# Optimization experiments

Measured on AMD Instinct MI355X. Metric: run time of the kernel, lower is better.

The kernel has to match this reference:

```python
import jax, jax.numpy as jnp
import numpy as np

D_MODEL = 1024
NUM_HEADS = 16
DEPTH = D_MODEL // NUM_HEADS
B, S = 2, 2048


def setup_inputs() -> dict:
    key = jax.random.key(0)
    ks = jax.random.split(key, 8)
    scale = 1.0 / np.sqrt(D_MODEL)
    return {
        "v": jax.random.normal(ks[0], (B, S, D_MODEL), jnp.float32),
        "k": jax.random.normal(ks[1], (B, S, D_MODEL), jnp.float32),
        "q": jax.random.normal(ks[2], (B, S, D_MODEL), jnp.float32),
        "mask": jnp.zeros((B, 1, 1, S), jnp.float32),
        "wq": jax.random.normal(ks[3], (D_MODEL, D_MODEL), jnp.float32) * scale,
        "wk": jax.random.normal(ks[4], (D_MODEL, D_MODEL), jnp.float32) * scale,
        "wv": jax.random.normal(ks[5], (D_MODEL, D_MODEL), jnp.float32) * scale,
        "wo": jax.random.normal(ks[6], (D_MODEL, D_MODEL), jnp.float32) * scale,
        "bq": jnp.zeros((D_MODEL,), jnp.float32),
        "bk": jnp.zeros((D_MODEL,), jnp.float32),
        "bv": jnp.zeros((D_MODEL,), jnp.float32),
        "bo": jnp.zeros((D_MODEL,), jnp.float32),
    }


def _split_heads(x):
    # [B, S, d_model] -> [B, H, S, depth]
    b, s, _ = x.shape
    return x.reshape(b, s, NUM_HEADS, DEPTH).transpose(0, 2, 1, 3)


def reference(v, k, q, mask, wq, wk, wv, wo, bq, bk, bv, bo):
    qh = _split_heads(q @ wq + bq)
    kh = _split_heads(k @ wk + bk)
    vh = _split_heads(v @ wv + bv)
    # scores: [B, H, Sq, Sk]
    scores = jnp.einsum("bhqd,bhkd->bhqk", qh, kh) / jnp.sqrt(
        jnp.asarray(DEPTH, jnp.float32))
    scores = scores + mask * -1e9
    attn = jax.nn.softmax(scores, axis=-1)
    out = jnp.einsum("bhqk,bhkd->bhqd", attn, vh)  # [B, H, Sq, depth]
    out = out.transpose(0, 2, 1, 3).reshape(q.shape[0], -1, D_MODEL)
    out = out @ wo + bo
    return out, attn
```

## Files before the change

kernel.cpp:

```cpp
#include <hip/hip_runtime.h>

#define S_LEN 2048
#define DM 1024
#define NH 16
#define DH 64

typedef __attribute__((ext_vector_type(8))) short short8;
typedef __attribute__((ext_vector_type(4))) float f32x4;
typedef __attribute__((ext_vector_type(16))) float f32x16;
typedef unsigned short u16;
typedef unsigned int u32;

__device__ __forceinline__ u16 f2b(float f){
  union { float f; u32 u; } v; v.f = f;
  return (u16)((v.u + 0x7fffu + ((v.u >> 16) & 1u)) >> 16);
}
__device__ __forceinline__ float b2f(u16 h){
  union { u32 u; float f; } v; v.u = ((u32)h) << 16; return v.f;
}

__device__ __forceinline__ f32x4 mfma16(short8 a, short8 b, f32x4 c){
  return __builtin_amdgcn_mfma_f32_16x16x32_bf16(a, b, c, 0, 0, 0);
}
__device__ __forceinline__ f32x16 mfma32(short8 a, short8 b, f32x16 c){
  return __builtin_amdgcn_mfma_f32_32x32x16_bf16(a, b, c, 0, 0, 0);
}

template<int R>
__device__ __forceinline__ void stage_tile(const u16* src, int ld, u16* lds){
  const int t = threadIdx.x;
  #pragma unroll
  for (int it = 0; it < R/32; ++it){
    int idx = it*256 + t;
    int row = idx >> 3;
    int ch  = (idx & 7) ^ (row & 7);
    const u16* g = src + row*ld + ch*8;
    u16* l = lds + (it*256 + (t & ~63))*8;
    __builtin_amdgcn_global_load_lds((const __attribute__((address_space(1))) void*)g,
                                     (__attribute__((address_space(3))) void*)l, 16, 0, 0);
  }
}

__device__ __forceinline__ short8 frag_ld(const u16* tile, int row, int ch){
  int off = (row*128 + ch*16) ^ ((row & 7) << 4);
  return *(const short8*)((const char*)tile + off);
}

__global__ __launch_bounds__(256) void k_cast(
    const float* __restrict__ q, const float* __restrict__ k, const float* __restrict__ v,
    u16* __restrict__ qb, u16* __restrict__ kb, u16* __restrict__ vb)
{
  int z = blockIdx.z;
  const float* src = (z==0)?q:(z==1)?k:v;
  u16* dst = (z==0)?qb:(z==1)?kb:vb;
  long i = ((long)blockIdx.x*256 + threadIdx.x)*8;
  f32x4 a = *(const f32x4*)(src + i);
  f32x4 b = *(const f32x4*)(src + i + 4);
  short8 o;
  #pragma unroll
  for (int j = 0; j < 4; ++j){ o[j] = (short)f2b(a[j]); o[4+j] = (short)f2b(b[j]); }
  *(short8*)(dst + i) = o;
}

__global__ __launch_bounds__(256) void k_transpose(
    const float* __restrict__ wq, const float* __restrict__ wk,
    const float* __restrict__ wv, const float* __restrict__ wo,
    u16* __restrict__ oq, u16* __restrict__ ok, u16* __restrict__ ov, u16* __restrict__ oo)
{
  int z = blockIdx.z;
  const float* W = (z==0)?wq:(z==1)?wk:(z==2)?wv:wo;
  u16* O = (z==0)?oq:(z==1)?ok:(z==2)?ov:oo;
  int k0 = blockIdx.x*64, n0 = blockIdx.y*64;
  __shared__ float tl[64][65];
  int t = threadIdx.x;
  #pragma unroll
  for (int i = 0; i < 16; ++i){
    int idx = i*256 + t;
    int row = idx >> 6, col = idx & 63;
    tl[row][col] = W[(long)(k0+row)*DM + n0 + col];
  }
  __syncthreads();
  #pragma unroll
  for (int i = 0; i < 16; ++i){
    int idx = i*256 + t;
    int n = idx >> 6, kk = idx & 63;
    O[(long)(n0+n)*DM + k0 + kk] = f2b(tl[kk][n]);
  }
}

__device__ __forceinline__ void gemm_body(const u16* __restrict__ X, const u16* __restrict__ WT,
    const float* __restrict__ bias, u16* __restrict__ dst16, float* __restrict__ dst32,
    int layout, int m0, int n0, u16* At, u16* Bt)
{
  const int t = threadIdx.x, lane = t & 63, w = t >> 6;
  const int wr = (w >> 1) * 64, wc = (w & 1) * 64;
  const int li = lane & 15, lg = lane >> 4;
  const f32x4 zero = {0.f, 0.f, 0.f, 0.f};
  f32x4 acc[4][4];
  #pragma unroll
  for (int m = 0; m < 4; ++m)
    #pragma unroll
    for (int n = 0; n < 4; ++n) acc[m][n] = zero;

  for (int kt = 0; kt < DM/64; ++kt){
    stage_tile<128>(X  + (long)m0*DM + kt*64, DM, At);
    stage_tile<128>(WT + (long)n0*DM + kt*64, DM, Bt);
    __syncthreads();
    #pragma unroll
    for (int ks = 0; ks < 2; ++ks){
      int ch = ks*4 + lg;
      short8 a[4], b[4];
      #pragma unroll
      for (int m = 0; m < 4; ++m) a[m] = frag_ld(At, wr + m*16 + li, ch);
      #pragma unroll
      for (int n = 0; n < 4; ++n) b[n] = frag_ld(Bt, wc + n*16 + li, ch);
      #pragma unroll
      for (int m = 0; m < 4; ++m)
        #pragma unroll
        for (int n = 0; n < 4; ++n) acc[m][n] = mfma16(a[m], b[n], acc[m][n]);
    }
    __syncthreads();
  }

  if (layout == 1){
    f32x4 bm[4];
    #pragma unroll
    for (int m = 0; m < 4; ++m) bm[m] = *(const f32x4*)(bias + m0 + wr + m*16 + lg*4);
    #pragma unroll
    for (int m = 0; m < 4; ++m)
      #pragma unroll
      for (int n = 0; n < 4; ++n)
        #pragma unroll
        for (int r = 0; r < 4; ++r){
          int gm = m0 + wr + m*16 + lg*4 + r;
          int gc = n0 + wc + n*16 + li;
          int hh = gm >> 6, dd = gm & 63, bb = gc >> 11, ss = gc & (S_LEN-1);
          dst16[(((long)(bb*NH + hh))*DH + dd)*S_LEN + ss] = f2b(acc[m][n][r] + bm[m][r]);
        }
  } else {
    float bv4[4];
    #pragma unroll
    for (int n = 0; n < 4; ++n) bv4[n] = bias[n0 + wc + n*16 + li];
    #pragma unroll
    for (int m = 0; m < 4; ++m)
      #pragma unroll
      for (int n = 0; n < 4; ++n)
        #pragma unroll
        for (int r = 0; r < 4; ++r){
          int gm = m0 + wr + m*16 + lg*4 + r;
          int gc = n0 + wc + n*16 + li;
          float val = acc[m][n][r] + bv4[n];
          if (layout == 0){
            int bb = gm >> 11, ss = gm & (S_LEN-1), hh = gc >> 6, dd = gc & 63;
            dst16[(((long)(bb*NH + hh))*S_LEN + ss)*DH + dd] = f2b(val);
          } else {
            dst32[(long)gm*DM + gc] = val;
          }
        }
  }
}

__global__ __launch_bounds__(256) void k_gemm_qkv(
    const u16* __restrict__ qb, const u16* __restrict__ kb, const u16* __restrict__ vb,
    const u16* __restrict__ wtq, const u16* __restrict__ wtk, const u16* __restrict__ wtv,
    const float* __restrict__ bq, const float* __restrict__ bk, const float* __restrict__ bv,
    u16* __restrict__ Qw, u16* __restrict__ Kw, u16* __restrict__ VTw)
{
  __shared__ u16 At[128*64], Bt[128*64];
  int bid = blockIdx.x;
  int xcd = bid & 7, j = bid >> 3;
  int z = j >> 5, tt = j & 31;
  int mi = xcd*4 + (tt >> 3), n = tt & 7;
  if (z == 2){
    gemm_body(wtv, vb, bv, VTw, nullptr, 1, n*128, mi*128, At, Bt);
  } else {
    const u16* X  = (z==0)?qb:kb;
    const u16* WT = (z==0)?wtq:wtk;
    const float* B = (z==0)?bq:bk;
    u16* dst = (z==0)?Qw:Kw;
    gemm_body(X, WT, B, dst, nullptr, 0, mi*128, n*128, At, Bt);
  }
}

__global__ __launch_bounds__(256) void k_gemm_out(
    const u16* __restrict__ ctx, const u16* __restrict__ wto,
    const float* __restrict__ bo, float* __restrict__ out)
{
  __shared__ u16 At[128*64], Bt[128*64];
  int bid = blockIdx.x;
  int xcd = bid & 7, tt = bid >> 3;
  int mi = xcd*4 + (tt >> 3), n = tt & 7;
  gemm_body(ctx, wto, bo, nullptr, out, 2, mi*128, n*128, At, Bt);
}

__global__ __launch_bounds__(256) void k_attn(const u16* __restrict__ Q, const u16* __restrict__ K,
    const u16* __restrict__ VT, const float* __restrict__ mask,
    float* __restrict__ attn, u16* __restrict__ ctx)
{
  __shared__ u16 Kt[2][64*64], Vt[2][64*64], Pt[128*64];
  const int t = threadIdx.x, lane = t & 63, w = t >> 6;
  const int lq = lane & 31, hi = lane >> 5;
  const int bid = blockIdx.x;
  const int bh = bid >> 4;
  const int q0 = (bid & 15) * 128;
  const int b = bh >> 4;
  const u16* Qb = Q + ((long)bh*S_LEN + q0 + w*32 + lq)*DH;
  short8 qa[4];
  #pragma unroll
  for (int ds = 0; ds < 4; ++ds) qa[ds] = *(const short8*)(Qb + ds*16 + hi*8);
  const float* mrow_g = mask + b*S_LEN;

  float lsum = 0.f;
  stage_tile<64>(K + (long)bh*S_LEN*DH, DH, Kt[0]);
  __syncthreads();
  for (int tt = 0; tt < S_LEN/64; ++tt){
    const u16* cur = Kt[tt & 1];
    if (tt + 1 < S_LEN/64)
      stage_tile<64>(K + ((long)bh*S_LEN + (tt+1)*64)*DH, DH, Kt[(tt+1) & 1]);
    #pragma unroll
    for (int kt = 0; kt < 2; ++kt){
      f32x16 acc = {};
      __builtin_amdgcn_s_setprio(1);
      #pragma unroll
      for (int ds = 0; ds < 4; ++ds)
        acc = mfma32(frag_ld(cur, kt*32 + lq, ds*2 + hi), qa[ds], acc);
      __builtin_amdgcn_s_setprio(0);
      #pragma unroll
      for (int rg = 0; rg < 4; ++rg){
        f32x4 mk = *(const f32x4*)(mrow_g + tt*64 + kt*32 + rg*8 + hi*4);
        #pragma unroll
        for (int j = 0; j < 4; ++j)
          lsum += __expf(acc[rg*4+j]*0.125f - 1e9f*mk[j]);
      }
    }
    __syncthreads();
  }
  lsum += __shfl_xor(lsum, 32);

  float rlw[8];
  #pragma unroll
  for (int i = 0; i < 8; ++i)
    rlw[i] = 1.f / __shfl(lsum, i*4 + (lane >> 4));

  f32x16 cacc[2] = {};
  const int prow = w*32 + lq;
  const int pswz = (prow & 7) << 4;

  stage_tile<64>(K  + (long)bh*S_LEN*DH, DH, Kt[0]);
  stage_tile<64>(VT + (long)bh*DH*S_LEN, S_LEN, Vt[0]);
  __syncthreads();
  for (int tt = 0; tt < S_LEN/64; ++tt){
    const int cur = tt & 1;
    if (tt + 1 < S_LEN/64){
      stage_tile<64>(K  + ((long)bh*S_LEN + (tt+1)*64)*DH, DH, Kt[cur^1]);
      stage_tile<64>(VT + (long)bh*DH*S_LEN + (tt+1)*64, S_LEN, Vt[cur^1]);
    }
    #pragma unroll
    for (int kt = 0; kt < 2; ++kt){
      f32x16 acc = {};
      __builtin_amdgcn_s_setprio(1);
      #pragma unroll
      for (int ds = 0; ds < 4; ++ds)
        acc = mfma32(frag_ld(Kt[cur], kt*32 + lq, ds*2 + hi), qa[ds], acc);
      __builtin_amdgcn_s_setprio(0);
      #pragma unroll
      for (int rg = 0; rg < 4; ++rg){
        f32x4 mk = *(const f32x4*)(mrow_g + tt*64 + kt*32 + rg*8 + hi*4);
        float p0 = __expf(acc[rg*4+0]*0.125f - 1e9f*mk[0]);
        float p1 = __expf(acc[rg*4+1]*0.125f - 1e9f*mk[1]);
        float p2 = __expf(acc[rg*4+2]*0.125f - 1e9f*mk[2]);
        float p3 = __expf(acc[rg*4+3]*0.125f - 1e9f*mk[3]);
        uint2 pu;
        pu.x = (u32)f2b(p0) | ((u32)f2b(p1) << 16);
        pu.y = (u32)f2b(p2) | ((u32)f2b(p3) << 16);
        int off = (prow*128 + (kt*32 + rg*8 + hi*4)*2) ^ pswz;
        *(uint2*)((char*)Pt + off) = pu;
      }
    }
    #pragma unroll
    for (int i = 0; i < 8; ++i){
      int rr = i*4 + (lane >> 4);
      int ch8 = lane & 15;
      int roff = ((w*32 + rr)*128 + ch8*8) ^ ((rr & 7) << 4);
      uint2 pr = *(const uint2*)((const char*)Pt + roff);
      f32x4 av;
      av[0] = b2f((u16)(pr.x & 0xffffu)) * rlw[i];
      av[1] = b2f((u16)(pr.x >> 16))     * rlw[i];
      av[2] = b2f((u16)(pr.y & 0xffffu)) * rlw[i];
      av[3] = b2f((u16)(pr.y >> 16))     * rlw[i];
      *(f32x4*)(attn + ((long)bh*S_LEN + q0 + w*32 + rr)*S_LEN + tt*64 + ch8*4) = av;
    }
    short8 pa[4];
    #pragma unroll
    for (int ks = 0; ks < 4; ++ks) pa[ks] = frag_ld(Pt, prow, ks*2 + hi);
    __builtin_amdgcn_s_setprio(1);
    #pragma unroll
    for (int dh = 0; dh < 2; ++dh)
      #pragma unroll
      for (int ks = 0; ks < 4; ++ks)
        cacc[dh] = mfma32(pa[ks], frag_ld(Vt[cur], dh*32 + lq, ks*2 + hi), cacc[dh]);
    __builtin_amdgcn_s_setprio(0);
    asm volatile("s_waitcnt vmcnt(8)" ::: "memory");
    __builtin_amdgcn_sched_barrier(0);
    __builtin_amdgcn_s_barrier();
  }

  int bb = bh >> 4, hh = bh & 15;
  #pragma unroll
  for (int r = 0; r < 16; ++r){
    int qrow = (r & 3) + 8*(r >> 2) + 4*hi;
    float rle = 1.f / __shfl(lsum, qrow);
    #pragma unroll
    for (int dh = 0; dh < 2; ++dh){
      float val = cacc[dh][r] * rle;
      ctx[((long)bb*S_LEN + q0 + w*32 + qrow)*DM + hh*DH + dh*32 + lq] = f2b(val);
    }
  }
}

extern "C" void kernel_launch(void* const* d_in, const int* in_sizes, int n_in,
                              void* d_out, int out_size, void* d_ws, size_t ws_size,
                              hipStream_t stream)
{
  const float* v_in = (const float*)d_in[0];
  const float* k_in = (const float*)d_in[1];
  const float* q_in = (const float*)d_in[2];
  const float* mask = (const float*)d_in[3];
  const float* wq = (const float*)d_in[4];
  const float* wk = (const float*)d_in[5];
  const float* wv = (const float*)d_in[6];
  const float* wo = (const float*)d_in[7];
  const float* bq = (const float*)d_in[8];
  const float* bk = (const float*)d_in[9];
  const float* bv = (const float*)d_in[10];
  const float* bo = (const float*)d_in[11];

  float* out  = (float*)d_out;
  float* attn = out + (long)2*S_LEN*DM;

  char* ws = (char*)d_ws;
  const long MW = 1024*1024;
  u16*  wtq = (u16*)(ws);
  u16*  wtk = (u16*)(ws + 2*MW);
  u16*  wtv = (u16*)(ws + 4*MW);
  u16*  wto = (u16*)(ws + 6*MW);
  u16*  qb  = (u16*)(ws + 8*MW);
  u16*  kb  = (u16*)(ws + 17*MW);
  u16*  vb  = (u16*)(ws + 26*MW);
  u16*  Qw  = (u16*)(ws + 35*MW);
  u16*  Kw  = (u16*)(ws + 44*MW);
  u16*  VTw = (u16*)(ws + 53*MW);
  u16*  ctx = (u16*)(ws + 8*MW);

  k_cast<<<dim3(2048,1,3), 256, 0, stream>>>(q_in, k_in, v_in, qb, kb, vb);
  k_transpose<<<dim3(16,16,4), 256, 0, stream>>>(wq,wk,wv,wo, wtq,wtk,wtv,wto);
  k_gemm_qkv<<<768, 256, 0, stream>>>(qb,kb,vb, wtq,wtk,wtv, bq,bk,bv, Qw,Kw,VTw);
  k_attn<<<512, 256, 0, stream>>>(Qw, Kw, VTw, mask, attn, ctx);
  k_gemm_out<<<256, 256, 0, stream>>>(ctx, wto, bo, out);
}
```

Measured before the change: 296.0 us.

## Load K/V fragments directly from global in attention, shrink blocks to two waves

The attention kernel no longer stages K and V tiles through shared memory with double buffering and barriers. Each wave now loads its MFMA fragments straight from global memory, relying on L2 for reuse. Blocks shrink to 128 threads covering 64 query rows, the grid doubles to 1024, and block ids are remapped so heads are grouped by XCD for L2 locality. This removes LDS traffic and block-wide syncs and raises occupancy, but each wave re-reads K/V from cache with less coalesced access and no explicit prefetch.

```diff
diff --git a/kernel.cpp b/kernel.cpp
--- a/kernel.cpp
+++ b/kernel.cpp
@@ -193,17 +193,20 @@
   gemm_body(ctx, wto, bo, nullptr, out, 2, mi*128, n*128, At, Bt);
 }
 
-__global__ __launch_bounds__(256) void k_attn(const u16* __restrict__ Q, const u16* __restrict__ K,
+__global__ __launch_bounds__(128) void k_attn(const u16* __restrict__ Q, const u16* __restrict__ K,
     const u16* __restrict__ VT, const float* __restrict__ mask,
     float* __restrict__ attn, u16* __restrict__ ctx)
 {
-  __shared__ u16 Kt[2][64*64], Vt[2][64*64], Pt[128*64];
+  __shared__ u16 Pt[64*64];
   const int t = threadIdx.x, lane = t & 63, w = t >> 6;
   const int lq = lane & 31, hi = lane >> 5;
   const int bid = blockIdx.x;
-  const int bh = bid >> 4;
-  const int q0 = (bid & 15) * 128;
+  const int xcd = bid & 7, j = bid >> 3;
+  const int bh = xcd + 8*(j & 3);
+  const int q0 = (j >> 2) * 64;
   const int b = bh >> 4;
+  const u16* Kb = K  + (long)bh*S_LEN*DH;
+  const u16* Vb = VT + (long)bh*DH*S_LEN;
   const u16* Qb = Q + ((long)bh*S_LEN + q0 + w*32 + lq)*DH;
   short8 qa[4];
   #pragma unroll
@@ -211,29 +214,26 @@
   const float* mrow_g = mask + b*S_LEN;
 
   float lsum = 0.f;
-  stage_tile<64>(K + (long)bh*S_LEN*DH, DH, Kt[0]);
-  __syncthreads();
   for (int tt = 0; tt < S_LEN/64; ++tt){
-    const u16* cur = Kt[tt & 1];
-    if (tt + 1 < S_LEN/64)
-      stage_tile<64>(K + ((long)bh*S_LEN + (tt+1)*64)*DH, DH, Kt[(tt+1) & 1]);
     #pragma unroll
     for (int kt = 0; kt < 2; ++kt){
+      short8 kf[4];
+      #pragma unroll
+      for (int ds = 0; ds < 4; ++ds)
+        kf[ds] = *(const short8*)(Kb + (long)(tt*64 + kt*32 + lq)*DH + ds*16 + hi*8);
       f32x16 acc = {};
       __builtin_amdgcn_s_setprio(1);
       #pragma unroll
-      for (int ds = 0; ds < 4; ++ds)
-        acc = mfma32(frag_ld(cur, kt*32 + lq, ds*2 + hi), qa[ds], acc);
+      for (int ds = 0; ds < 4; ++ds) acc = mfma32(kf[ds], qa[ds], acc);
       __builtin_amdgcn_s_setprio(0);
       #pragma unroll
       for (int rg = 0; rg < 4; ++rg){
         f32x4 mk = *(const f32x4*)(mrow_g + tt*64 + kt*32 + rg*8 + hi*4);
         #pragma unroll
-        for (int j = 0; j < 4; ++j)
-          lsum += __expf(acc[rg*4+j]*0.125f - 1e9f*mk[j]);
+        for (int jj = 0; jj < 4; ++jj)
+          lsum += __expf(acc[rg*4+jj]*0.125f - 1e9f*mk[jj]);
       }
     }
-    __syncthreads();
   }
   lsum += __shfl_xor(lsum, 32);
 
@@ -246,22 +246,17 @@
   const int prow = w*32 + lq;
   const int pswz = (prow & 7) << 4;
 
-  stage_tile<64>(K  + (long)bh*S_LEN*DH, DH, Kt[0]);
-  stage_tile<64>(VT + (long)bh*DH*S_LEN, S_LEN, Vt[0]);
-  __syncthreads();
   for (int tt = 0; tt < S_LEN/64; ++tt){
-    const int cur = tt & 1;
-    if (tt + 1 < S_LEN/64){
-      stage_tile<64>(K  + ((long)bh*S_LEN + (tt+1)*64)*DH, DH, Kt[cur^1]);
-      stage_tile<64>(VT + (long)bh*DH*S_LEN + (tt+1)*64, S_LEN, Vt[cur^1]);
-    }
     #pragma unroll
     for (int kt = 0; kt < 2; ++kt){
+      short8 kf[4];
+      #pragma unroll
+      for (int ds = 0; ds < 4; ++ds)
+        kf[ds] = *(const short8*)(Kb + (long)(tt*64 + kt*32 + lq)*DH + ds*16 + hi*8);
       f32x16 acc = {};
       __builtin_amdgcn_s_setprio(1);
       #pragma unroll
-      for (int ds = 0; ds < 4; ++ds)
-        acc = mfma32(frag_ld(Kt[cur], kt*32 + lq, ds*2 + hi), qa[ds], acc);
+      for (int ds = 0; ds < 4; ++ds) acc = mfma32(kf[ds], qa[ds], acc);
       __builtin_amdgcn_s_setprio(0);
       #pragma unroll
       for (int rg = 0; rg < 4; ++rg){
@@ -293,16 +288,19 @@
     short8 pa[4];
     #pragma unroll
     for (int ks = 0; ks < 4; ++ks) pa[ks] = frag_ld(Pt, prow, ks*2 + hi);
+    short8 vf[2][4];
+    #pragma unroll
+    for (int dh = 0; dh < 2; ++dh)
+      #pragma unroll
+      for (int ks = 0; ks < 4; ++ks)
+        vf[dh][ks] = *(const short8*)(Vb + (long)(dh*32 + lq)*S_LEN + tt*64 + ks*16 + hi*8);
     __builtin_amdgcn_s_setprio(1);
     #pragma unroll
     for (int dh = 0; dh < 2; ++dh)
       #pragma unroll
       for (int ks = 0; ks < 4; ++ks)
-        cacc[dh] = mfma32(pa[ks], frag_ld(Vt[cur], dh*32 + lq, ks*2 + hi), cacc[dh]);
+        cacc[dh] = mfma32(pa[ks], vf[dh][ks], cacc[dh]);
     __builtin_amdgcn_s_setprio(0);
-    asm volatile("s_waitcnt vmcnt(8)" ::: "memory");
-    __builtin_amdgcn_sched_barrier(0);
-    __builtin_amdgcn_s_barrier();
   }
 
   int bb = bh >> 4, hh = bh & 15;
@@ -355,6 +353,6 @@
   k_cast<<<dim3(2048,1,3), 256, 0, stream>>>(q_in, k_in, v_in, qb, kb, vb);
   k_transpose<<<dim3(16,16,4), 256, 0, stream>>>(wq,wk,wv,wo, wtq,wtk,wtv,wto);
   k_gemm_qkv<<<768, 256, 0, stream>>>(qb,kb,vb, wtq,wtk,wtv, bq,bk,bv, Qw,Kw,VTw);
-  k_attn<<<512, 256, 0, stream>>>(Qw, Kw, VTw, mask, attn, ctx);
+  k_attn<<<1024, 128, 0, stream>>>(Qw, Kw, VTw, mask, attn, ctx);
   k_gemm_out<<<256, 256, 0, stream>>>(ctx, wto, bo, out);
 }
```

Result: slower. 377.1 us (+27.4%).

## Process two 32-row query groups per wave to reuse K/V fragments in attention

Applied to the files above, without the earlier changes.

Each wave now computes 64 query rows as two 32-row groups, loading each K and V fragment from LDS once and feeding it into two MFMA chains. Block size in queries doubles, so the grid halves to 256 blocks, and blocks are remapped so each XCD serves a fixed set of heads for L2 locality. This cuts LDS fragment loads and K/V tile restaging per query, at the cost of more registers, a larger P buffer in LDS, and fewer resident blocks to hide memory latency.

```diff
diff --git a/kernel.cpp b/kernel.cpp
--- a/kernel.cpp
+++ b/kernel.cpp
@@ -197,20 +197,24 @@
     const u16* __restrict__ VT, const float* __restrict__ mask,
     float* __restrict__ attn, u16* __restrict__ ctx)
 {
-  __shared__ u16 Kt[2][64*64], Vt[2][64*64], Pt[128*64];
+  __shared__ u16 Kt[2][64*64], Vt[2][64*64], Pt[256*64];
   const int t = threadIdx.x, lane = t & 63, w = t >> 6;
   const int lq = lane & 31, hi = lane >> 5;
   const int bid = blockIdx.x;
-  const int bh = bid >> 4;
-  const int q0 = (bid & 15) * 128;
+  const int xcd = bid & 7, j = bid >> 3;
+  const int bh = xcd + 8*(j & 3);
+  const int q0 = (j >> 2) * 256;
   const int b = bh >> 4;
-  const u16* Qb = Q + ((long)bh*S_LEN + q0 + w*32 + lq)*DH;
-  short8 qa[4];
-  #pragma unroll
-  for (int ds = 0; ds < 4; ++ds) qa[ds] = *(const short8*)(Qb + ds*16 + hi*8);
+  short8 qa[2][4];
+  #pragma unroll
+  for (int g = 0; g < 2; ++g){
+    const u16* Qb = Q + ((long)bh*S_LEN + q0 + w*64 + g*32 + lq)*DH;
+    #pragma unroll
+    for (int ds = 0; ds < 4; ++ds) qa[g][ds] = *(const short8*)(Qb + ds*16 + hi*8);
+  }
   const float* mrow_g = mask + b*S_LEN;
 
-  float lsum = 0.f;
+  float lsum0 = 0.f, lsum1 = 0.f;
   stage_tile<64>(K + (long)bh*S_LEN*DH, DH, Kt[0]);
   __syncthreads();
   for (int tt = 0; tt < S_LEN/64; ++tt){
@@ -219,32 +223,42 @@
       stage_tile<64>(K + ((long)bh*S_LEN + (tt+1)*64)*DH, DH, Kt[(tt+1) & 1]);
     #pragma unroll
     for (int kt = 0; kt < 2; ++kt){
-      f32x16 acc = {};
+      short8 kf[4];
+      #pragma unroll
+      for (int ds = 0; ds < 4; ++ds) kf[ds] = frag_ld(cur, kt*32 + lq, ds*2 + hi);
+      f32x16 a0 = {}, a1 = {};
       __builtin_amdgcn_s_setprio(1);
       #pragma unroll
-      for (int ds = 0; ds < 4; ++ds)
-        acc = mfma32(frag_ld(cur, kt*32 + lq, ds*2 + hi), qa[ds], acc);
+      for (int ds = 0; ds < 4; ++ds) a0 = mfma32(kf[ds], qa[0][ds], a0);
+      #pragma unroll
+      for (int ds = 0; ds < 4; ++ds) a1 = mfma32(kf[ds], qa[1][ds], a1);
       __builtin_amdgcn_s_setprio(0);
       #pragma unroll
       for (int rg = 0; rg < 4; ++rg){
         f32x4 mk = *(const f32x4*)(mrow_g + tt*64 + kt*32 + rg*8 + hi*4);
         #pragma unroll
-        for (int j = 0; j < 4; ++j)
-          lsum += __expf(acc[rg*4+j]*0.125f - 1e9f*mk[j]);
+        for (int jj = 0; jj < 4; ++jj){
+          lsum0 += __expf(a0[rg*4+jj]*0.125f - 1e9f*mk[jj]);
+          lsum1 += __expf(a1[rg*4+jj]*0.125f - 1e9f*mk[jj]);
+        }
       }
     }
     __syncthreads();
   }
-  lsum += __shfl_xor(lsum, 32);
-
-  float rlw[8];
-  #pragma unroll
-  for (int i = 0; i < 8; ++i)
-    rlw[i] = 1.f / __shfl(lsum, i*4 + (lane >> 4));
-
-  f32x16 cacc[2] = {};
-  const int prow = w*32 + lq;
-  const int pswz = (prow & 7) << 4;
+  lsum0 += __shfl_xor(lsum0, 32);
+  lsum1 += __shfl_xor(lsum1, 32);
+
+  float rlw[16];
+  #pragma unroll
+  for (int i = 0; i < 16; ++i){
+    float ls = (i < 8) ? lsum0 : lsum1;
+    rlw[i] = 1.f / __shfl(ls, (i*4 + (lane >> 4)) & 31);
+  }
+
+  f32x16 cacc[2][2] = {};
+  const int prow0 = w*64 + lq;
+  const int prow1 = w*64 + 32 + lq;
+  const int pswz = (lq & 7) << 4;
 
   stage_tile<64>(K  + (long)bh*S_LEN*DH, DH, Kt[0]);
   stage_tile<64>(VT + (long)bh*DH*S_LEN, S_LEN, Vt[0]);
@@ -257,65 +271,94 @@
     }
     #pragma unroll
     for (int kt = 0; kt < 2; ++kt){
-      f32x16 acc = {};
+      short8 kf[4];
+      #pragma unroll
+      for (int ds = 0; ds < 4; ++ds) kf[ds] = frag_ld(Kt[cur], kt*32 + lq, ds*2 + hi);
+      f32x16 a0 = {}, a1 = {};
       __builtin_amdgcn_s_setprio(1);
       #pragma unroll
-      for (int ds = 0; ds < 4; ++ds)
-        acc = mfma32(frag_ld(Kt[cur], kt*32 + lq, ds*2 + hi), qa[ds], acc);
+      for (int ds = 0; ds < 4; ++ds) a0 = mfma32(kf[ds], qa[0][ds], a0);
+      #pragma unroll
+      for (int ds = 0; ds < 4; ++ds) a1 = mfma32(kf[ds], qa[1][ds], a1);
       __builtin_amdgcn_s_setprio(0);
       #pragma unroll
       for (int rg = 0; rg < 4; ++rg){
         f32x4 mk = *(const f32x4*)(mrow_g + tt*64 + kt*32 + rg*8 + hi*4);
-        float p0 = __expf(acc[rg*4+0]*0.125f - 1e9f*mk[0]);
-        float p1 = __expf(acc[rg*4+1]*0.125f - 1e9f*mk[1]);
-        float p2 = __expf(acc[rg*4+2]*0.125f - 1e9f*mk[2]);
-        float p3 = __expf(acc[rg*4+3]*0.125f - 1e9f*mk[3]);
-        uint2 pu;
-        pu.x = (u32)f2b(p0) | ((u32)f2b(p1) << 16);
-        pu.y = (u32)f2b(p2) | ((u32)f2b(p3) << 16);
-        int off = (prow*128 + (kt*32 + rg*8 + hi*4)*2) ^ pswz;
-        *(uint2*)((char*)Pt + off) = pu;
+        int koff = (kt*32 + rg*8 + hi*4)*2;
+        {
+          float p0 = __expf(a0[rg*4+0]*0.125f - 1e9f*mk[0]);
+          float p1 = __expf(a0[rg*4+1]*0.125f - 1e9f*mk[1]);
+          float p2 = __expf(a0[rg*4+2]*0.125f - 1e9f*mk[2]);
+          float p3 = __expf(a0[rg*4+3]*0.125f - 1e9f*mk[3]);
+          uint2 pu;
+          pu.x = (u32)f2b(p0) | ((u32)f2b(p1) << 16);
+          pu.y = (u32)f2b(p2) | ((u32)f2b(p3) << 16);
+          *(uint2*)((char*)Pt + ((prow0*128 + koff) ^ pswz)) = pu;
+        }
+        {
+          float p0 = __expf(a1[rg*4+0]*0.125f - 1e9f*mk[0]);
+          float p1 = __expf(a1[rg*4+1]*0.125f - 1e9f*mk[1]);
+          float p2 = __expf(a1[rg*4+2]*0.125f - 1e9f*mk[2]);
+          float p3 = __expf(a1[rg*4+3]*0.125f - 1e9f*mk[3]);
+          uint2 pu;
+          pu.x = (u32)f2b(p0) | ((u32)f2b(p1) << 16);
+          pu.y = (u32)f2b(p2) | ((u32)f2b(p3) << 16);
+          *(uint2*)((char*)Pt + ((prow1*128 + koff) ^ pswz)) = pu;
+        }
       }
     }
     #pragma unroll
-    for (int i = 0; i < 8; ++i){
+    for (int i = 0; i < 16; ++i){
       int rr = i*4 + (lane >> 4);
       int ch8 = lane & 15;
-      int roff = ((w*32 + rr)*128 + ch8*8) ^ ((rr & 7) << 4);
+      int roff = ((w*64 + rr)*128 + ch8*8) ^ ((rr & 7) << 4);
       uint2 pr = *(const uint2*)((const char*)Pt + roff);
       f32x4 av;
       av[0] = b2f((u16)(pr.x & 0xffffu)) * rlw[i];
       av[1] = b2f((u16)(pr.x >> 16))     * rlw[i];
       av[2] = b2f((u16)(pr.y & 0xffffu)) * rlw[i];
       av[3] = b2f((u16)(pr.y >> 16))     * rlw[i];
-      *(f32x4*)(attn + ((long)bh*S_LEN + q0 + w*32 + rr)*S_LEN + tt*64 + ch8*4) = av;
-    }
-    short8 pa[4];
-    #pragma unroll
-    for (int ks = 0; ks < 4; ++ks) pa[ks] = frag_ld(Pt, prow, ks*2 + hi);
+      *(f32x4*)(attn + ((long)bh*S_LEN + q0 + w*64 + rr)*S_LEN + tt*64 + ch8*4) = av;
+    }
+    short8 vf[2][4];
+    #pragma unroll
+    for (int dh = 0; dh < 2; ++dh)
+      #pragma unroll
+      for (int ks = 0; ks < 4; ++ks)
+        vf[dh][ks] = frag_ld(Vt[cur], dh*32 + lq, ks*2 + hi);
+    short8 pa0[4], pa1[4];
+    #pragma unroll
+    for (int ks = 0; ks < 4; ++ks){
+      pa0[ks] = frag_ld(Pt, prow0, ks*2 + hi);
+      pa1[ks] = frag_ld(Pt, prow1, ks*2 + hi);
+    }
     __builtin_amdgcn_s_setprio(1);
     #pragma unroll
     for (int dh = 0; dh < 2; ++dh)
       #pragma unroll
-      for (int ks = 0; ks < 4; ++ks)
-        cacc[dh] = mfma32(pa[ks], frag_ld(Vt[cur], dh*32 + lq, ks*2 + hi), cacc[dh]);
+      for (int ks = 0; ks < 4; ++ks){
+        cacc[0][dh] = mfma32(pa0[ks], vf[dh][ks], cacc[0][dh]);
+        cacc[1][dh] = mfma32(pa1[ks], vf[dh][ks], cacc[1][dh]);
+      }
     __builtin_amdgcn_s_setprio(0);
-    asm volatile("s_waitcnt vmcnt(8)" ::: "memory");
+    asm volatile("s_waitcnt vmcnt(16)" ::: "memory");
     __builtin_amdgcn_sched_barrier(0);
     __builtin_amdgcn_s_barrier();
   }
 
   int bb = bh >> 4, hh = bh & 15;
   #pragma unroll
-  for (int r = 0; r < 16; ++r){
-    int qrow = (r & 3) + 8*(r >> 2) + 4*hi;
-    float rle = 1.f / __shfl(lsum, qrow);
-    #pragma unroll
-    for (int dh = 0; dh < 2; ++dh){
-      float val = cacc[dh][r] * rle;
-      ctx[((long)bb*S_LEN + q0 + w*32 + qrow)*DM + hh*DH + dh*32 + lq] = f2b(val);
-    }
-  }
+  for (int g = 0; g < 2; ++g)
+    #pragma unroll
+    for (int r = 0; r < 16; ++r){
+      int qrow = (r & 3) + 8*(r >> 2) + 4*hi;
+      float rle = 1.f / __shfl(g ? lsum1 : lsum0, qrow);
+      #pragma unroll
+      for (int dh = 0; dh < 2; ++dh){
+        float val = cacc[g][dh][r] * rle;
+        ctx[((long)bb*S_LEN + q0 + w*64 + g*32 + qrow)*DM + hh*DH + dh*32 + lq] = f2b(val);
+      }
+    }
 }
 
 extern "C" void kernel_launch(void* const* d_in, const int* in_sizes, int n_in,
@@ -355,6 +398,6 @@
   k_cast<<<dim3(2048,1,3), 256, 0, stream>>>(q_in, k_in, v_in, qb, kb, vb);
   k_transpose<<<dim3(16,16,4), 256, 0, stream>>>(wq,wk,wv,wo, wtq,wtk,wtv,wto);
   k_gemm_qkv<<<768, 256, 0, stream>>>(qb,kb,vb, wtq,wtk,wtv, bq,bk,bv, Qw,Kw,VTw);
-  k_attn<<<512, 256, 0, stream>>>(Qw, Kw, VTw, mask, attn, ctx);
+  k_attn<<<256, 256, 0, stream>>>(Qw, Kw, VTw, mask, attn, ctx);
   k_gemm_out<<<256, 256, 0, stream>>>(ctx, wto, bo, out);
 }
```

After: 347.6 us. +17.5%, slower.

## Split attention row-sum pass into separate high-parallelism kernel with key-halves

Applied to the files above, without the earlier changes.

Moves the softmax denominator pass out of the main attention kernel into k_attn1. That kernel runs 2048 blocks of 128 threads, each summing exp over half the keys for 64 query rows, and writes partial sums to the workspace. The main attention kernel then reads the two partials instead of recomputing them, uses an XCD-aware block mapping, and reads a mask that is premultiplied by -1e9 in a tiny kernel. The aim is to raise occupancy and parallelism for the first pass. The cost is two extra launches and the global traffic for the partial sums, and K is still read twice.

```diff
diff --git a/kernel.cpp b/kernel.cpp
--- a/kernel.cpp
+++ b/kernel.cpp
@@ -26,16 +26,16 @@
   return __builtin_amdgcn_mfma_f32_32x32x16_bf16(a, b, c, 0, 0, 0);
 }
 
-template<int R>
+template<int R, int NT>
 __device__ __forceinline__ void stage_tile(const u16* src, int ld, u16* lds){
   const int t = threadIdx.x;
   #pragma unroll
-  for (int it = 0; it < R/32; ++it){
-    int idx = it*256 + t;
+  for (int it = 0; it < R*8/NT; ++it){
+    int idx = it*NT + t;
     int row = idx >> 3;
     int ch  = (idx & 7) ^ (row & 7);
     const u16* g = src + row*ld + ch*8;
-    u16* l = lds + (it*256 + (t & ~63))*8;
+    u16* l = lds + (it*NT + (t & ~63))*8;
     __builtin_amdgcn_global_load_lds((const __attribute__((address_space(1))) void*)g,
                                      (__attribute__((address_space(3))) void*)l, 16, 0, 0);
   }
@@ -62,6 +62,13 @@
   *(short8*)(dst + i) = o;
 }
 
+__global__ __launch_bounds__(256) void k_maskb(const float* __restrict__ mask,
+                                               float* __restrict__ maskb)
+{
+  int i = blockIdx.x*256 + threadIdx.x;
+  maskb[i] = -1e9f * mask[i];
+}
+
 __global__ __launch_bounds__(256) void k_transpose(
     const float* __restrict__ wq, const float* __restrict__ wk,
     const float* __restrict__ wv, const float* __restrict__ wo,
@@ -103,8 +110,8 @@
     for (int n = 0; n < 4; ++n) acc[m][n] = zero;
 
   for (int kt = 0; kt < DM/64; ++kt){
-    stage_tile<128>(X  + (long)m0*DM + kt*64, DM, At);
-    stage_tile<128>(WT + (long)n0*DM + kt*64, DM, Bt);
+    stage_tile<128,256>(X  + (long)m0*DM + kt*64, DM, At);
+    stage_tile<128,256>(WT + (long)n0*DM + kt*64, DM, Bt);
     __syncthreads();
     #pragma unroll
     for (int ks = 0; ks < 2; ++ks){
@@ -193,67 +200,98 @@
   gemm_body(ctx, wto, bo, nullptr, out, 2, mi*128, n*128, At, Bt);
 }
 
-__global__ __launch_bounds__(256) void k_attn(const u16* __restrict__ Q, const u16* __restrict__ K,
-    const u16* __restrict__ VT, const float* __restrict__ mask,
-    float* __restrict__ attn, u16* __restrict__ ctx)
+__global__ __launch_bounds__(128) void k_attn1(const u16* __restrict__ Q,
+    const u16* __restrict__ K, const float* __restrict__ maskb,
+    float* __restrict__ lp0, float* __restrict__ lp1)
+{
+  __shared__ u16 Kt[2][64*64];
+  const int t = threadIdx.x, lane = t & 63, w = t >> 6;
+  const int lq = lane & 31, hi = lane >> 5;
+  const int bid = blockIdx.x;
+  const int xcd = bid & 7, j = bid >> 3;
+  const int kh = j & 1, jj = j >> 1;
+  const int bh = xcd + 8*(jj & 3);
+  const int q0 = (jj >> 2) * 64;
+  const int b = bh >> 4;
+  const int k0 = kh * (S_LEN/2);
+  const u16* Qb = Q + ((long)bh*S_LEN + q0 + w*32 + lq)*DH;
+  short8 qa[4];
+  #pragma unroll
+  for (int ds = 0; ds < 4; ++ds) qa[ds] = *(const short8*)(Qb + ds*16 + hi*8);
+  const float* mb_g = maskb + b*S_LEN + k0;
+  const u16* Kb = K + ((long)bh*S_LEN + k0)*DH;
+
+  float lsum = 0.f;
+  stage_tile<64,128>(Kb, DH, Kt[0]);
+  __syncthreads();
+  for (int tt = 0; tt < S_LEN/128; ++tt){
+    const u16* cur = Kt[tt & 1];
+    if (tt + 1 < S_LEN/128)
+      stage_tile<64,128>(Kb + (long)(tt+1)*64*DH, DH, Kt[(tt+1) & 1]);
+    #pragma unroll
+    for (int kt = 0; kt < 2; ++kt){
+      f32x16 acc = {};
+      __builtin_amdgcn_s_setprio(1);
+      #pragma unroll
+      for (int ds = 0; ds < 4; ++ds)
+        acc = mfma32(frag_ld(cur, kt*32 + lq, ds*2 + hi), qa[ds], acc);
+      __builtin_amdgcn_s_setprio(0);
+      #pragma unroll
+      for (int rg = 0; rg < 4; ++rg){
+        f32x4 mb = *(const f32x4*)(mb_g + tt*64 + kt*32 + rg*8 + hi*4);
+        #pragma unroll
+        for (int jj2 = 0; jj2 < 4; ++jj2)
+          lsum += __expf(acc[rg*4+jj2]*0.125f + mb[jj2]);
+      }
+    }
+    __syncthreads();
+  }
+  lsum += __shfl_xor(lsum, 32);
+  if (hi == 0){
+    float* lp = kh ? lp1 : lp0;
+    lp[bh*S_LEN + q0 + w*32 + lq] = lsum;
+  }
+}
+
+__global__ __launch_bounds__(256) void k_attn2(const u16* __restrict__ Q,
+    const u16* __restrict__ K, const u16* __restrict__ VT,
+    const float* __restrict__ maskb, const float* __restrict__ lp0,
+    const float* __restrict__ lp1, float* __restrict__ attn, u16* __restrict__ ctx)
 {
   __shared__ u16 Kt[2][64*64], Vt[2][64*64], Pt[128*64];
   const int t = threadIdx.x, lane = t & 63, w = t >> 6;
   const int lq = lane & 31, hi = lane >> 5;
   const int bid = blockIdx.x;
-  const int bh = bid >> 4;
-  const int q0 = (bid & 15) * 128;
+  const int xcd = bid & 7, j = bid >> 3;
+  const int bh = xcd + 8*(j & 3);
+  const int q0 = (j >> 2) * 128;
   const int b = bh >> 4;
   const u16* Qb = Q + ((long)bh*S_LEN + q0 + w*32 + lq)*DH;
   short8 qa[4];
   #pragma unroll
   for (int ds = 0; ds < 4; ++ds) qa[ds] = *(const short8*)(Qb + ds*16 + hi*8);
-  const float* mrow_g = mask + b*S_LEN;
-
-  float lsum = 0.f;
-  stage_tile<64>(K + (long)bh*S_LEN*DH, DH, Kt[0]);
-  __syncthreads();
-  for (int tt = 0; tt < S_LEN/64; ++tt){
-    const u16* cur = Kt[tt & 1];
-    if (tt + 1 < S_LEN/64)
-      stage_tile<64>(K + ((long)bh*S_LEN + (tt+1)*64)*DH, DH, Kt[(tt+1) & 1]);
-    #pragma unroll
-    for (int kt = 0; kt < 2; ++kt){
-      f32x16 acc = {};
-      __builtin_amdgcn_s_setprio(1);
-      #pragma unroll
-      for (int ds = 0; ds < 4; ++ds)
-        acc = mfma32(frag_ld(cur, kt*32 + lq, ds*2 + hi), qa[ds], acc);
-      __builtin_amdgcn_s_setprio(0);
-      #pragma unroll
-      for (int rg = 0; rg < 4; ++rg){
-        f32x4 mk = *(const f32x4*)(mrow_g + tt*64 + kt*32 + rg*8 + hi*4);
-        #pragma unroll
-        for (int j = 0; j < 4; ++j)
-          lsum += __expf(acc[rg*4+j]*0.125f - 1e9f*mk[j]);
-      }
-    }
-    __syncthreads();
-  }
-  lsum += __shfl_xor(lsum, 32);
+  const float* mb_g = maskb + b*S_LEN;
+  const long lbase = (long)bh*S_LEN + q0 + w*32;
 
   float rlw[8];
   #pragma unroll
-  for (int i = 0; i < 8; ++i)
-    rlw[i] = 1.f / __shfl(lsum, i*4 + (lane >> 4));
+  for (int i = 0; i < 8; ++i){
+    int qq = i*4 + (lane >> 4);
+    rlw[i] = 1.f / (lp0[lbase + qq] + lp1[lbase + qq]);
+  }
 
   f32x16 cacc[2] = {};
   const int prow = w*32 + lq;
   const int pswz = (prow & 7) << 4;
 
-  stage_tile<64>(K  + (long)bh*S_LEN*DH, DH, Kt[0]);
-  stage_tile<64>(VT + (long)bh*DH*S_LEN, S_LEN, Vt[0]);
+  stage_tile<64,256>(K  + (long)bh*S_LEN*DH, DH, Kt[0]);
+  stage_tile<64,256>(VT + (long)bh*DH*S_LEN, S_LEN, Vt[0]);
   __syncthreads();
   for (int tt = 0; tt < S_LEN/64; ++tt){
     const int cur = tt & 1;
     if (tt + 1 < S_LEN/64){
-      stage_tile<64>(K  + ((long)bh*S_LEN + (tt+1)*64)*DH, DH, Kt[cur^1]);
-      stage_tile<64>(VT + (long)bh*DH*S_LEN + (tt+1)*64, S_LEN, Vt[cur^1]);
+      stage_tile<64,256>(K  + ((long)bh*S_LEN + (tt+1)*64)*DH, DH, Kt[cur^1]);
+      stage_tile<64,256>(VT + (long)bh*DH*S_LEN + (tt+1)*64, S_LEN, Vt[cur^1]);
     }
     #pragma unroll
     for (int kt = 0; kt < 2; ++kt){
@@ -265,11 +303,11 @@
       __builtin_amdgcn_s_setprio(0);
       #pragma unroll
       for (int rg = 0; rg < 4; ++rg){
-        f32x4 mk = *(const f32x4*)(mrow_g + tt*64 + kt*32 + rg*8 + hi*4);
-        float p0 = __expf(acc[rg*4+0]*0.125f - 1e9f*mk[0]);
-        float p1 = __expf(acc[rg*4+1]*0.125f - 1e9f*mk[1]);
-        float p2 = __expf(acc[rg*4+2]*0.125f - 1e9f*mk[2]);
-        float p3 = __expf(acc[rg*4+3]*0.125f - 1e9f*mk[3]);
+        f32x4 mb = *(const f32x4*)(mb_g + tt*64 + kt*32 + rg*8 + hi*4);
+        float p0 = __expf(acc[rg*4+0]*0.125f + mb[0]);
+        float p1 = __expf(acc[rg*4+1]*0.125f + mb[1]);
+        float p2 = __expf(acc[rg*4+2]*0.125f + mb[2]);
+        float p3 = __expf(acc[rg*4+3]*0.125f + mb[3]);
         uint2 pu;
         pu.x = (u32)f2b(p0) | ((u32)f2b(p1) << 16);
         pu.y = (u32)f2b(p2) | ((u32)f2b(p3) << 16);
@@ -309,7 +347,7 @@
   #pragma unroll
   for (int r = 0; r < 16; ++r){
     int qrow = (r & 3) + 8*(r >> 2) + 4*hi;
-    float rle = 1.f / __shfl(lsum, qrow);
+    float rle = 1.f / (lp0[lbase - w*32 + w*32 + qrow] + lp1[lbase + qrow]);
     #pragma unroll
     for (int dh = 0; dh < 2; ++dh){
       float val = cacc[dh][r] * rle;
@@ -351,10 +389,15 @@
   u16*  Kw  = (u16*)(ws + 44*MW);
   u16*  VTw = (u16*)(ws + 53*MW);
   u16*  ctx = (u16*)(ws + 8*MW);
+  float* lp0   = (float*)(ws + 62*MW);
+  float* lp1   = (float*)(ws + 62*MW + 262144);
+  float* maskb = (float*)(ws + 63*MW);
 
   k_cast<<<dim3(2048,1,3), 256, 0, stream>>>(q_in, k_in, v_in, qb, kb, vb);
+  k_maskb<<<16, 256, 0, stream>>>(mask, maskb);
   k_transpose<<<dim3(16,16,4), 256, 0, stream>>>(wq,wk,wv,wo, wtq,wtk,wtv,wto);
   k_gemm_qkv<<<768, 256, 0, stream>>>(qb,kb,vb, wtq,wtk,wtv, bq,bk,bv, Qw,Kw,VTw);
-  k_attn<<<512, 256, 0, stream>>>(Qw, Kw, VTw, mask, attn, ctx);
+  k_attn1<<<2048, 128, 0, stream>>>(Qw, Kw, maskb, lp0, lp1);
+  k_attn2<<<512, 256, 0, stream>>>(Qw, Kw, VTw, maskb, lp0, lp1, attn, ctx);
   k_gemm_out<<<256, 256, 0, stream>>>(ctx, wto, bo, out);
 }
```

Measured after the change: 294.9 us. Within noise of the previous version (-0.3%).
